# Kernel optimization log

Measured on AMD Instinct MI355X. Metric: run time of the kernel, lower is better.

## Reference

```python
import jax, jax.numpy as jnp
import numpy as np

D_MODEL = 1024
NUM_HEADS = 16
HEAD_DIM = D_MODEL // NUM_HEADS
B, L = 2, 2048


def setup_inputs() -> dict:
    key = jax.random.key(0)
    ks = jax.random.split(key, 11)
    s = 1.0 / np.sqrt(D_MODEL)
    return {
        "query": jax.random.normal(ks[0], (B, L, D_MODEL), jnp.float32),
        "key": jax.random.normal(ks[1], (B, L, D_MODEL), jnp.float32),
        "value": jax.random.normal(ks[2], (B, L, D_MODEL), jnp.float32),
        "Wq": jax.random.uniform(ks[3], (D_MODEL, D_MODEL), jnp.float32, -s, s),
        "bq": jax.random.uniform(ks[4], (D_MODEL,), jnp.float32, -s, s),
        "Wk": jax.random.uniform(ks[5], (D_MODEL, D_MODEL), jnp.float32, -s, s),
        "bk": jax.random.uniform(ks[6], (D_MODEL,), jnp.float32, -s, s),
        "Wv": jax.random.uniform(ks[7], (D_MODEL, D_MODEL), jnp.float32, -s, s),
        "bv": jax.random.uniform(ks[8], (D_MODEL,), jnp.float32, -s, s),
        "Wo": jax.random.uniform(ks[9], (D_MODEL, D_MODEL), jnp.float32, -s, s),
        "bo": jax.random.uniform(ks[10], (D_MODEL,), jnp.float32, -s, s),
    }


def _split_heads(x):
    b, l, _ = x.shape
    return x.reshape(b, l, NUM_HEADS, HEAD_DIM).transpose(0, 2, 1, 3)  # [B,H,L,Dh]


def reference(query, key, value, Wq, bq, Wk, bk, Wv, bv, Wo, bo):
    Q = _split_heads(query @ Wq.T + bq)
    K = _split_heads(key @ Wk.T + bk)
    V = _split_heads(value @ Wv.T + bv)
    scores = jnp.einsum('bhqd,bhkd->bhqk', Q, K) / jnp.sqrt(jnp.float32(HEAD_DIM))
    attn = jax.nn.softmax(scores, axis=-1)
    ctx = jnp.einsum('bhqk,bhkd->bhqd', attn, V)  # [B,H,L,Dh]
    b, h, l, dh = ctx.shape
    merged = ctx.transpose(0, 2, 1, 3).reshape(b, l, h * dh)
    return merged @ Wo.T + bo
```

## Files before the change

### kernel.cpp

```cpp
#include <hip/hip_runtime.h>

#define B_   2
#define L_   2048
#define D_   1024
#define H_   16
#define DH_  64
#define T_   (B_ * L_)

typedef __bf16 bf16x8 __attribute__((ext_vector_type(8)));
typedef float f32x4 __attribute__((ext_vector_type(4)));
typedef unsigned int u32x4 __attribute__((ext_vector_type(4)));
typedef unsigned short u16x4 __attribute__((ext_vector_type(4)));
typedef unsigned short u16x8 __attribute__((ext_vector_type(8)));

static __device__ __forceinline__ unsigned short f2bf(float x) {
  unsigned int u = __float_as_uint(x);
  u += 0x7fffu + ((u >> 16) & 1u);
  return (unsigned short)(u >> 16);
}

static __device__ __forceinline__ bf16x8 ld_bf8(const unsigned short* p) {
  return __builtin_bit_cast(bf16x8, *reinterpret_cast<const u32x4*>(p));
}

static __device__ __forceinline__ void async_cp16(const unsigned short* g, unsigned short* l) {
  __builtin_amdgcn_global_load_lds(
      (const __attribute__((address_space(1))) unsigned int*)g,
      (__attribute__((address_space(3))) unsigned int*)l,
      16, 0, 0);
}

__global__ void convert_bf16_all(
    const float* __restrict__ q, const float* __restrict__ k, const float* __restrict__ v,
    const float* __restrict__ wq, const float* __restrict__ wk, const float* __restrict__ wv,
    const float* __restrict__ wo, unsigned short* __restrict__ ws) {
  const int M1 = 1 << 20;
  const float* src;
  unsigned short* dst;
  int n;
  switch (blockIdx.y) {
    case 0: src = wq; dst = ws;           n = M1;     break;
    case 1: src = wk; dst = ws + M1;      n = M1;     break;
    case 2: src = wv; dst = ws + 2 * M1;  n = M1;     break;
    case 3: src = wo; dst = ws + 3 * M1;  n = M1;     break;
    case 4: src = q;  dst = ws + 4 * M1;  n = 4 * M1; break;
    case 5: src = k;  dst = ws + 8 * M1;  n = 4 * M1; break;
    default: src = v; dst = ws + 12 * M1; n = 4 * M1; break;
  }
  int i = (blockIdx.x * 256 + threadIdx.x) * 8;
  if (i >= n) return;
  float4 a = *reinterpret_cast<const float4*>(src + i);
  float4 b = *reinterpret_cast<const float4*>(src + i + 4);
  u16x8 o;
  o[0] = f2bf(a.x); o[1] = f2bf(a.y); o[2] = f2bf(a.z); o[3] = f2bf(a.w);
  o[4] = f2bf(b.x); o[5] = f2bf(b.y); o[6] = f2bf(b.z); o[7] = f2bf(b.w);
  *reinterpret_cast<u16x8*>(dst + i) = o;
}

template <int NF>
static __device__ __forceinline__ void gemm_db(
    const unsigned short* __restrict__ A, const unsigned short* __restrict__ Bw,
    int K, int brow, int bcol, unsigned short* As, unsigned short* Bs,
    f32x4 (&acc)[4][NF]) {
  constexpr int BSZ = NF * 1024;
  const int t = threadIdx.x;
  const int lane = t & 63;
  const int wid = t >> 6;
  const int wr = (wid >> 1) << 6;
  const int wc = (wid & 1) * (NF * 16);
  const int lrow = lane & 15;
  const int lko = (lane >> 4) << 3;
  const int r2 = t >> 2;
  const int c8 = (t & 3) << 3;
  const int so = t * 8;

  f32x4 zero = {0.f, 0.f, 0.f, 0.f};
#pragma unroll
  for (int i = 0; i < 4; ++i)
#pragma unroll
    for (int n = 0; n < NF; ++n) acc[i][n] = zero;

  const unsigned short* ga = A + (size_t)(brow + r2) * K + c8;
  const unsigned short* gb = Bw + (size_t)(bcol + r2) * K + c8;

  async_cp16(ga,                  &As[so]);
  async_cp16(ga + (size_t)64 * K, &As[2048 + so]);
  async_cp16(gb,                  &Bs[so]);
  if constexpr (NF == 4) async_cp16(gb + (size_t)64 * K, &Bs[2048 + so]);
  __syncthreads();

  int cur = 0;
  for (int k0 = 0; k0 < K; k0 += 32) {
    const int nx = (k0 + 32 < K) ? k0 + 32 : 0;
    unsigned short* Asn = &As[(cur ^ 1) * 4096];
    unsigned short* Bsn = &Bs[(cur ^ 1) * BSZ];
    async_cp16(ga + nx,                  &Asn[so]);
    async_cp16(ga + (size_t)64 * K + nx, &Asn[2048 + so]);
    async_cp16(gb + nx,                  &Bsn[so]);
    if constexpr (NF == 4) async_cp16(gb + (size_t)64 * K + nx, &Bsn[2048 + so]);

    const unsigned short* Asc = &As[cur * 4096];
    const unsigned short* Bsc = &Bs[cur * BSZ];
    bf16x8 af[4], bfr[NF];
#pragma unroll
    for (int i = 0; i < 4; ++i) af[i] = ld_bf8(&Asc[(wr + i * 16 + lrow) * 32 + lko]);
#pragma unroll
    for (int n = 0; n < NF; ++n) bfr[n] = ld_bf8(&Bsc[(wc + n * 16 + lrow) * 32 + lko]);
#pragma unroll
    for (int i = 0; i < 4; ++i)
#pragma unroll
      for (int n = 0; n < NF; ++n)
        acc[i][n] = __builtin_amdgcn_mfma_f32_16x16x32_bf16(af[i], bfr[n], acc[i][n], 0, 0, 0);

    __syncthreads();
    cur ^= 1;
  }
}

__global__ void proj_qkv(
    const unsigned short* __restrict__ xq, const unsigned short* __restrict__ xk,
    const unsigned short* __restrict__ xv, const unsigned short* __restrict__ wqb,
    const unsigned short* __restrict__ wkb, const unsigned short* __restrict__ wvb,
    const float* __restrict__ bq, const float* __restrict__ bk, const float* __restrict__ bv,
    unsigned short* __restrict__ Qb, unsigned short* __restrict__ Kb,
    unsigned short* __restrict__ Vt) {
  __shared__ unsigned short As[2 * 4096], Bs[2 * 4096];
  const int z = blockIdx.z;
  const unsigned short* A = (z == 0) ? xq : (z == 1) ? xk : xv;
  const unsigned short* W = (z == 0) ? wqb : (z == 1) ? wkb : wvb;
  const float* bias = (z == 0) ? bq : (z == 1) ? bk : bv;
  const int brow = blockIdx.x * 128, bcol = blockIdx.y * 128;

  f32x4 acc[4][4];
  gemm_db<4>(A, W, D_, brow, bcol, As, Bs, acc);

  const int lane = threadIdx.x & 63;
  const int wid = threadIdx.x >> 6;
  const int wr = (wid >> 1) << 6, wc = (wid & 1) << 6;
  const int lcol = lane & 15, lr4 = (lane >> 4) << 2;

  if (z < 2) {
    unsigned short* Dst = (z == 0) ? Qb : Kb;
    const float scl = (z == 0) ? 0.125f : 1.0f;
#pragma unroll
    for (int i = 0; i < 4; ++i)
#pragma unroll
      for (int n = 0; n < 4; ++n) {
        const int col = bcol + wc + n * 16 + lcol;
        const float bb = bias[col];
        const int h = col >> 6, dh = col & 63;
#pragma unroll
        for (int j = 0; j < 4; ++j) {
          const int row = brow + wr + i * 16 + lr4 + j;
          const int batch = row >> 11, ll = row & 2047;
          Dst[(((size_t)(batch * H_ + h) * L_) + ll) * DH_ + dh] =
              f2bf((acc[i][n][j] + bb) * scl);
        }
      }
  } else {
#pragma unroll
    for (int i = 0; i < 4; ++i)
#pragma unroll
    for (int n = 0; n < 4; ++n) {
        const int col = bcol + wc + n * 16 + lcol;
        const float bb = bias[col];
        const int h = col >> 6, dh = col & 63;
        const int row0 = brow + wr + i * 16 + lr4;
        const int batch = row0 >> 11, ll = row0 & 2047;
        u16x4 pk;
#pragma unroll
        for (int j = 0; j < 4; ++j) pk[j] = f2bf(acc[i][n][j] + bb);
        *reinterpret_cast<u16x4*>(
            &Vt[((size_t)((batch * H_ + h) * DH_ + dh)) * L_ + ll]) = pk;
      }
  }
}

__global__ __launch_bounds__(256, 4) void attn_fwd(
    const unsigned short* __restrict__ Qb,
    const unsigned short* __restrict__ Kb,
    const unsigned short* __restrict__ Vt,
    unsigned short* __restrict__ ctx) {
  __shared__ unsigned short Ks[2][64 * 64];
  __shared__ unsigned short Vs[2][64 * 64];
  __shared__ unsigned short Ps[4][16 * 64];
  const int t = threadIdx.x;
  const int wid = t >> 6, lane = t & 63;
  const int bh = blockIdx.y;
  const int q0 = blockIdx.x * 64 + wid * 16;
  const int lcol = lane & 15;
  const int hi = lane >> 4;
  const int lk = hi << 3;
  const int lr4 = hi << 2;
  const int sxl = (lcol & 7) << 3;

  const unsigned short* Qh = Qb + (size_t)bh * L_ * DH_;
  const unsigned short* Kh = Kb + (size_t)bh * L_ * DH_;
  const unsigned short* Vh = Vt + (size_t)bh * DH_ * L_;

  const int so = t * 8;
  const int sr = t >> 3;
  const int ssw = ((t & 7) * 8) ^ ((sr & 7) << 3);

  bf16x8 qf[2];
#pragma unroll
  for (int kk = 0; kk < 2; ++kk)
    qf[kk] = ld_bf8(Qh + (size_t)(q0 + lcol) * DH_ + kk * 32 + lk);

  bf16x8 ones;
#pragma unroll
  for (int i = 0; i < 8; ++i) ones[i] = (__bf16)1.0f;

  f32x4 zero = {0.f, 0.f, 0.f, 0.f};
  f32x4 o[4];
#pragma unroll
  for (int n = 0; n < 4; ++n) o[n] = zero;
  f32x4 lsum = zero;

  async_cp16(Kh + (size_t)sr * DH_ + ssw,        &Ks[0][so]);
  async_cp16(Kh + (size_t)(sr + 32) * DH_ + ssw, &Ks[0][so + 2048]);
  async_cp16(Vh + (size_t)sr * L_ + ssw,         &Vs[0][so]);
  async_cp16(Vh + (size_t)(sr + 32) * L_ + ssw,  &Vs[0][so + 2048]);
  __syncthreads();

  int cur = 0;
  for (int kv = 0; kv < L_; kv += 64) {
    const int nx = (kv + 64 < L_) ? kv + 64 : 0;
    async_cp16(Kh + (size_t)(nx + sr) * DH_ + ssw,      &Ks[cur ^ 1][so]);
    async_cp16(Kh + (size_t)(nx + sr + 32) * DH_ + ssw, &Ks[cur ^ 1][so + 2048]);
    async_cp16(Vh + (size_t)sr * L_ + nx + ssw,         &Vs[cur ^ 1][so]);
    async_cp16(Vh + (size_t)(sr + 32) * L_ + nx + ssw,  &Vs[cur ^ 1][so + 2048]);

    f32x4 s[4];
#pragma unroll
    for (int n = 0; n < 4; ++n) s[n] = zero;
#pragma unroll
    for (int n = 0; n < 4; ++n)
#pragma unroll
      for (int kk = 0; kk < 2; ++kk) {
        bf16x8 kf = ld_bf8(&Ks[cur][(n * 16 + lcol) * 64 + ((kk * 32 + lk) ^ sxl)]);
        s[n] = __builtin_amdgcn_mfma_f32_16x16x32_bf16(qf[kk], kf, s[n], 0, 0, 0);
      }

#pragma unroll
    for (int n = 0; n < 4; ++n)
#pragma unroll
      for (int j = 0; j < 4; ++j) {
        const int r = lr4 + j;
        Ps[wid][r * 64 + ((n * 16 + lcol) ^ ((r & 7) << 3))] = f2bf(__expf(s[n][j]));
      }

    bf16x8 pf[2];
#pragma unroll
    for (int kk = 0; kk < 2; ++kk)
      pf[kk] = ld_bf8(&Ps[wid][lcol * 64 + ((kk * 32 + lk) ^ sxl)]);

#pragma unroll
    for (int kk = 0; kk < 2; ++kk)
      lsum = __builtin_amdgcn_mfma_f32_16x16x32_bf16(pf[kk], ones, lsum, 0, 0, 0);

#pragma unroll
    for (int kk = 0; kk < 2; ++kk)
#pragma unroll
      for (int n = 0; n < 4; ++n) {
        bf16x8 vf = ld_bf8(&Vs[cur][(n * 16 + lcol) * 64 + ((kk * 32 + lk) ^ sxl)]);
        o[n] = __builtin_amdgcn_mfma_f32_16x16x32_bf16(pf[kk], vf, o[n], 0, 0, 0);
      }

    __syncthreads();
    cur ^= 1;
  }

  const int b = bh >> 4, h = bh & 15;
#pragma unroll
  for (int j = 0; j < 4; ++j) {
    const float inv = 1.0f / lsum[j];
    const int lq = q0 + lr4 + j;
#pragma unroll
    for (int n = 0; n < 4; ++n) {
      const int c = h * DH_ + n * 16 + lcol;
      ctx[((size_t)(b * L_ + lq)) * D_ + c] = f2bf(o[n][j] * inv);
    }
  }
}

__global__ void out_proj(const unsigned short* __restrict__ ctx,
                         const unsigned short* __restrict__ wob,
                         const float* __restrict__ bo, float* __restrict__ out) {
  __shared__ unsigned short As[2 * 4096], Bs[2 * 2048];
  const int brow = blockIdx.x * 128, bcol = blockIdx.y * 64;
  f32x4 acc[4][2];
  gemm_db<2>(ctx, wob, D_, brow, bcol, As, Bs, acc);

  const int lane = threadIdx.x & 63;
  const int wid = threadIdx.x >> 6;
  const int wr = (wid >> 1) << 6, wc = (wid & 1) << 5;
  const int lcol = lane & 15, lr4 = (lane >> 4) << 2;
#pragma unroll
  for (int i = 0; i < 4; ++i)
#pragma unroll
    for (int n = 0; n < 2; ++n) {
      const int col = bcol + wc + n * 16 + lcol;
      const float bb = bo[col];
#pragma unroll
      for (int j = 0; j < 4; ++j) {
        const int row = brow + wr + i * 16 + lr4 + j;
        out[(size_t)row * D_ + col] = acc[i][n][j] + bb;
      }
    }
}

extern "C" void kernel_launch(void* const* d_in, const int* in_sizes, int n_in,
                              void* d_out, int out_size, void* d_ws, size_t ws_size,
                              hipStream_t stream) {
  (void)in_sizes; (void)n_in; (void)out_size; (void)ws_size;
  const float* q  = (const float*)d_in[0];
  const float* k  = (const float*)d_in[1];
  const float* v  = (const float*)d_in[2];
  const float* bq = (const float*)d_in[4];
  const float* bk = (const float*)d_in[6];
  const float* bv = (const float*)d_in[8];
  const float* bo = (const float*)d_in[10];
  const float* Wq = (const float*)d_in[3];
  const float* Wk = (const float*)d_in[5];
  const float* Wv = (const float*)d_in[7];
  const float* Wo = (const float*)d_in[9];

  unsigned short* w = (unsigned short*)d_ws;
  const size_t M1 = 1u << 20;
  unsigned short* wqb = w;
  unsigned short* wkb = w + M1;
  unsigned short* wvb = w + 2 * M1;
  unsigned short* wob = w + 3 * M1;
  unsigned short* xq  = w + 4 * M1;
  unsigned short* xk  = w + 8 * M1;
  unsigned short* xv  = w + 12 * M1;
  unsigned short* Qb  = w + 16 * M1;
  unsigned short* Kb  = w + 20 * M1;
  unsigned short* Vt  = w + 24 * M1;
  unsigned short* ctx = w + 28 * M1;
  float* out = (float*)d_out;

  convert_bf16_all<<<dim3(2048, 7), dim3(256), 0, stream>>>(q, k, v, Wq, Wk, Wv, Wo, w);
  proj_qkv<<<dim3(T_ / 128, D_ / 128, 3), dim3(256), 0, stream>>>(
      xq, xk, xv, wqb, wkb, wvb, bq, bk, bv, Qb, Kb, Vt);
  attn_fwd<<<dim3(L_ / 64, B_ * H_), dim3(256), 0, stream>>>(Qb, Kb, Vt, ctx);
  out_proj<<<dim3(T_ / 128, D_ / 64), dim3(256), 0, stream>>>(ctx, wob, bo, out);
}
```

Before: 231.2 us.

## Process two 16-row query groups per wave in attention to reuse K/V tiles

Each wave in the attention kernel now handles 32 query rows instead of 16, so every block covers 128 queries and the grid halves. Each K and V fragment read from shared memory feeds two MFMAs, which halves shared-memory traffic and global K/V loads per query. The cost is doubled accumulator registers, launch bounds lowered to 2 blocks per SM, a larger P buffer, and fewer blocks in total (512), which may reduce occupancy and latency hiding.

```diff
diff --git a/kernel.cpp b/kernel.cpp
--- a/kernel.cpp
+++ b/kernel.cpp
@@ -161,7 +161,7 @@
 #pragma unroll
     for (int i = 0; i < 4; ++i)
 #pragma unroll
-    for (int n = 0; n < 4; ++n) {
+      for (int n = 0; n < 4; ++n) {
         const int col = bcol + wc + n * 16 + lcol;
         const float bb = bias[col];
         const int h = col >> 6, dh = col & 63;
@@ -176,18 +176,18 @@
   }
 }
 
-__global__ __launch_bounds__(256, 4) void attn_fwd(
+__global__ __launch_bounds__(256, 2) void attn_fwd(
     const unsigned short* __restrict__ Qb,
     const unsigned short* __restrict__ Kb,
     const unsigned short* __restrict__ Vt,
     unsigned short* __restrict__ ctx) {
   __shared__ unsigned short Ks[2][64 * 64];
   __shared__ unsigned short Vs[2][64 * 64];
-  __shared__ unsigned short Ps[4][16 * 64];
+  __shared__ unsigned short Ps[4][32 * 64];
   const int t = threadIdx.x;
   const int wid = t >> 6, lane = t & 63;
   const int bh = blockIdx.y;
-  const int q0 = blockIdx.x * 64 + wid * 16;
+  const int q0 = blockIdx.x * 128 + wid * 32;
   const int lcol = lane & 15;
   const int hi = lane >> 4;
   const int lk = hi << 3;
@@ -202,20 +202,24 @@
   const int sr = t >> 3;
   const int ssw = ((t & 7) * 8) ^ ((sr & 7) << 3);
 
-  bf16x8 qf[2];
-#pragma unroll
-  for (int kk = 0; kk < 2; ++kk)
-    qf[kk] = ld_bf8(Qh + (size_t)(q0 + lcol) * DH_ + kk * 32 + lk);
+  bf16x8 qf[2][2];
+#pragma unroll
+  for (int rg = 0; rg < 2; ++rg)
+#pragma unroll
+    for (int kk = 0; kk < 2; ++kk)
+      qf[rg][kk] = ld_bf8(Qh + (size_t)(q0 + rg * 16 + lcol) * DH_ + kk * 32 + lk);
 
   bf16x8 ones;
 #pragma unroll
   for (int i = 0; i < 8; ++i) ones[i] = (__bf16)1.0f;
 
   f32x4 zero = {0.f, 0.f, 0.f, 0.f};
-  f32x4 o[4];
-#pragma unroll
-  for (int n = 0; n < 4; ++n) o[n] = zero;
-  f32x4 lsum = zero;
+  f32x4 o[2][4];
+#pragma unroll
+  for (int rg = 0; rg < 2; ++rg)
+#pragma unroll
+    for (int n = 0; n < 4; ++n) o[rg][n] = zero;
+  f32x4 lsum[2] = {zero, zero};
 
   async_cp16(Kh + (size_t)sr * DH_ + ssw,        &Ks[0][so]);
   async_cp16(Kh + (size_t)(sr + 32) * DH_ + ssw, &Ks[0][so + 2048]);
@@ -223,6 +227,7 @@
   async_cp16(Vh + (size_t)(sr + 32) * L_ + ssw,  &Vs[0][so + 2048]);
   __syncthreads();
 
+  unsigned short* Pw = &Ps[wid][0];
   int cur = 0;
   for (int kv = 0; kv < L_; kv += 64) {
     const int nx = (kv + 64 < L_) ? kv + 64 : 0;
@@ -231,40 +236,50 @@
     async_cp16(Vh + (size_t)sr * L_ + nx + ssw,         &Vs[cur ^ 1][so]);
     async_cp16(Vh + (size_t)(sr + 32) * L_ + nx + ssw,  &Vs[cur ^ 1][so + 2048]);
 
-    f32x4 s[4];
-#pragma unroll
-    for (int n = 0; n < 4; ++n) s[n] = zero;
+    f32x4 s[2][4];
+#pragma unroll
+    for (int rg = 0; rg < 2; ++rg)
+#pragma unroll
+      for (int n = 0; n < 4; ++n) s[rg][n] = zero;
 #pragma unroll
     for (int n = 0; n < 4; ++n)
 #pragma unroll
       for (int kk = 0; kk < 2; ++kk) {
         bf16x8 kf = ld_bf8(&Ks[cur][(n * 16 + lcol) * 64 + ((kk * 32 + lk) ^ sxl)]);
-        s[n] = __builtin_amdgcn_mfma_f32_16x16x32_bf16(qf[kk], kf, s[n], 0, 0, 0);
-      }
-
-#pragma unroll
-    for (int n = 0; n < 4; ++n)
-#pragma unroll
-      for (int j = 0; j < 4; ++j) {
-        const int r = lr4 + j;
-        Ps[wid][r * 64 + ((n * 16 + lcol) ^ ((r & 7) << 3))] = f2bf(__expf(s[n][j]));
-      }
-
-    bf16x8 pf[2];
-#pragma unroll
-    for (int kk = 0; kk < 2; ++kk)
-      pf[kk] = ld_bf8(&Ps[wid][lcol * 64 + ((kk * 32 + lk) ^ sxl)]);
-
-#pragma unroll
-    for (int kk = 0; kk < 2; ++kk)
-      lsum = __builtin_amdgcn_mfma_f32_16x16x32_bf16(pf[kk], ones, lsum, 0, 0, 0);
+        s[0][n] = __builtin_amdgcn_mfma_f32_16x16x32_bf16(qf[0][kk], kf, s[0][n], 0, 0, 0);
+        s[1][n] = __builtin_amdgcn_mfma_f32_16x16x32_bf16(qf[1][kk], kf, s[1][n], 0, 0, 0);
+      }
+
+#pragma unroll
+    for (int rg = 0; rg < 2; ++rg)
+#pragma unroll
+      for (int n = 0; n < 4; ++n)
+#pragma unroll
+        for (int j = 0; j < 4; ++j) {
+          const int r = rg * 16 + lr4 + j;
+          Pw[r * 64 + ((n * 16 + lcol) ^ ((r & 7) << 3))] = f2bf(__expf(s[rg][n][j]));
+        }
+
+    bf16x8 pf[2][2];
+#pragma unroll
+    for (int rg = 0; rg < 2; ++rg)
+#pragma unroll
+      for (int kk = 0; kk < 2; ++kk)
+        pf[rg][kk] = ld_bf8(&Pw[(rg * 16 + lcol) * 64 + ((kk * 32 + lk) ^ sxl)]);
+
+#pragma unroll
+    for (int rg = 0; rg < 2; ++rg)
+#pragma unroll
+      for (int kk = 0; kk < 2; ++kk)
+        lsum[rg] = __builtin_amdgcn_mfma_f32_16x16x32_bf16(pf[rg][kk], ones, lsum[rg], 0, 0, 0);
 
 #pragma unroll
     for (int kk = 0; kk < 2; ++kk)
 #pragma unroll
       for (int n = 0; n < 4; ++n) {
         bf16x8 vf = ld_bf8(&Vs[cur][(n * 16 + lcol) * 64 + ((kk * 32 + lk) ^ sxl)]);
-        o[n] = __builtin_amdgcn_mfma_f32_16x16x32_bf16(pf[kk], vf, o[n], 0, 0, 0);
+        o[0][n] = __builtin_amdgcn_mfma_f32_16x16x32_bf16(pf[0][kk], vf, o[0][n], 0, 0, 0);
+        o[1][n] = __builtin_amdgcn_mfma_f32_16x16x32_bf16(pf[1][kk], vf, o[1][n], 0, 0, 0);
       }
 
     __syncthreads();
@@ -273,15 +288,17 @@
 
   const int b = bh >> 4, h = bh & 15;
 #pragma unroll
-  for (int j = 0; j < 4; ++j) {
-    const float inv = 1.0f / lsum[j];
-    const int lq = q0 + lr4 + j;
-#pragma unroll
-    for (int n = 0; n < 4; ++n) {
-      const int c = h * DH_ + n * 16 + lcol;
-      ctx[((size_t)(b * L_ + lq)) * D_ + c] = f2bf(o[n][j] * inv);
+  for (int rg = 0; rg < 2; ++rg)
+#pragma unroll
+    for (int j = 0; j < 4; ++j) {
+      const float inv = 1.0f / lsum[rg][j];
+      const int lq = q0 + rg * 16 + lr4 + j;
+#pragma unroll
+      for (int n = 0; n < 4; ++n) {
+        const int c = h * DH_ + n * 16 + lcol;
+        ctx[((size_t)(b * L_ + lq)) * D_ + c] = f2bf(o[rg][n][j] * inv);
+      }
     }
-  }
 }
 
 __global__ void out_proj(const unsigned short* __restrict__ ctx,
@@ -344,6 +361,6 @@
   convert_bf16_all<<<dim3(2048, 7), dim3(256), 0, stream>>>(q, k, v, Wq, Wk, Wv, Wo, w);
   proj_qkv<<<dim3(T_ / 128, D_ / 128, 3), dim3(256), 0, stream>>>(
       xq, xk, xv, wqb, wkb, wvb, bq, bk, bv, Qb, Kb, Vt);
-  attn_fwd<<<dim3(L_ / 64, B_ * H_), dim3(256), 0, stream>>>(Qb, Kb, Vt, ctx);
+  attn_fwd<<<dim3(L_ / 128, B_ * H_), dim3(256), 0, stream>>>(Qb, Kb, Vt, ctx);
   out_proj<<<dim3(T_ / 128, D_ / 64), dim3(256), 0, stream>>>(ctx, wob, bo, out);
 }
```

Measured after the change: 233.5 us. No clear change (+1.0%).
